# Kernel tuning notes

Measured on AMD Instinct MI355X. Metric: run time of the kernel, lower is better.

The kernel has to match this reference:

```python
import math
import jax, jax.numpy as jnp
import numpy as np

B, T, D = 4, 4096, 2048
D_MEM, H, D_HEAD = 1024, 16, 64
TABLE = 131072          # rows per head
K, DIL = 4, 2           # kernel_size, dilation = max_ngram
EPS_QK = float(np.finfo(np.float32).eps)  # nn.RMSNorm default eps
EPS_CONV = 1e-5


def _rmsnorm(x, gamma, eps):
    ms = jnp.mean(jnp.square(x), axis=-1, keepdims=True)
    return x * jax.lax.rsqrt(ms + eps) * gamma


def setup_inputs() -> dict:
    key = jax.random.key(0)
    ks = jax.random.split(key, 8)
    hidden_states = jax.random.normal(ks[0], (B, T, D), dtype=jnp.float32)
    hash_ids = jax.random.randint(ks[1], (B, T, H), 0, TABLE, dtype=jnp.int32)
    emb_table = jax.random.normal(ks[2], (H * TABLE, D_HEAD), dtype=jnp.float32) * 0.02
    key_W = jax.random.normal(ks[3], (D, D_MEM), dtype=jnp.float32) * (1.0 / math.sqrt(D_MEM))
    key_b = jnp.zeros((D,), dtype=jnp.float32)
    value_W = jax.random.normal(ks[4], (D, D_MEM), dtype=jnp.float32) * (1.0 / math.sqrt(D_MEM))
    value_b = jnp.zeros((D,), dtype=jnp.float32)
    q_gamma = jnp.ones((D,), dtype=jnp.float32)
    k_gamma = jnp.ones((D,), dtype=jnp.float32)
    cnorm_gamma = jnp.ones((D,), dtype=jnp.float32)
    conv_w = jax.random.normal(ks[5], (D, 1, K), dtype=jnp.float32) * 0.1
    return dict(hidden_states=hidden_states, hash_ids=hash_ids, emb_table=emb_table,
                key_W=key_W, key_b=key_b, value_W=value_W, value_b=value_b,
                q_gamma=q_gamma, k_gamma=k_gamma, cnorm_gamma=cnorm_gamma, conv_w=conv_w)


def reference(hidden_states, hash_ids, emb_table, key_W, key_b, value_W, value_b,
              q_gamma, k_gamma, cnorm_gamma, conv_w):
    # --- MultiHeadEmbedding: per-head offset into a single fused table ---
    offsets = (jnp.arange(H, dtype=hash_ids.dtype) * TABLE)  # [H]
    shifted = hash_ids + offsets                              # [B,T,H]
    e = emb_table[shifted].reshape(B, T, D_MEM)               # gather + flatten heads

    # --- key / value projections (torch Linear: x @ W.T + b) ---
    k = jnp.einsum('btm,dm->btd', e, key_W) + key_b
    v = jnp.einsum('btm,dm->btd', e, value_W) + value_b

    # --- RMSNorm q and k, dot-product gate (in fp32, demo mode) ---
    qn = _rmsnorm(hidden_states, q_gamma, EPS_QK)
    kn = _rmsnorm(k, k_gamma, EPS_QK)
    dot = jnp.sum(qn * kn, axis=-1) / math.sqrt(D)            # [B,T]
    dot = jnp.sqrt(jnp.maximum(jnp.abs(dot), 1e-6)) * jnp.sign(dot)  # demo gating
    gate = jax.nn.sigmoid(dot)[..., None]                     # [B,T,1]
    gated_v = gate * v                                        # [B,T,D]

    # --- ShortDepthwiseCausalConv: RMSNorm -> depthwise causal conv -> SiLU ---
    yn = _rmsnorm(gated_v, cnorm_gamma, EPS_CONV)
    yn_t = jnp.transpose(yn, (0, 2, 1))                       # [B,D,T]
    left_pad = (K - 1) * DIL
    yc = jax.lax.conv_general_dilated(
        yn_t, conv_w, window_strides=(1,), padding=[(left_pad, 0)],
        rhs_dilation=(DIL,), feature_group_count=D,
        dimension_numbers=('NCH', 'OIH', 'NCH'))              # [B,D,T]
    y = jnp.transpose(jax.nn.silu(yc), (0, 2, 1))             # [B,T,D]
    return y + gated_v
```

## Files before the change

### kernel.cpp

```cpp
#include <hip/hip_runtime.h>
#include <hip/hip_bf16.h>
#include <math.h>

#define B_      4
#define T_      4096
#define D_      2048
#define DMEM_   1024
#define H_      16
#define TABLE_  131072
#define NTOK    (B_ * T_)
#define NKV     (2 * D_)
#define NT_TILES 16
#define EPS_QK  1.1920928955078125e-07f
#define EPS_CONV 1e-5f
#define INV_D   (1.0f / 2048.0f)
#define INV_SQRT_D 0.02209708691207961f

typedef __attribute__((ext_vector_type(8))) __bf16 bf16x8;
typedef __attribute__((ext_vector_type(4))) float  f32x4;
typedef __attribute__((ext_vector_type(8))) unsigned short u16x8;

typedef __attribute__((address_space(3))) unsigned int       lds_u32;
typedef const __attribute__((address_space(1))) unsigned int glb_u32;

__device__ __forceinline__ unsigned short f2bf(float f) {
    unsigned u = __float_as_uint(f);
    u += 0x7fff + ((u >> 16) & 1);
    return (unsigned short)(u >> 16);
}
__device__ __forceinline__ float bf2f(unsigned short u) {
    return __uint_as_float(((unsigned)u) << 16);
}
__device__ __forceinline__ void gload16(const void* g, void* l) {
    __builtin_amdgcn_global_load_lds((glb_u32*)g, (lds_u32*)l, 16, 0, 0);
}

#define DSHR(x, n) __int_as_float(__builtin_amdgcn_update_dpp( \
    0, __float_as_int(x), 0x110 + (n), 0xf, 0xf, false))
#define RED16(x) do { x += DSHR(x, 1); x += DSHR(x, 2); \
                      x += DSHR(x, 4); x += DSHR(x, 8); } while (0)

__global__ __launch_bounds__(256) void prep(
    const int* __restrict__ hash_ids, const float* __restrict__ table,
    const float* __restrict__ kW, const float* __restrict__ vW,
    const float* __restrict__ kb, const float* __restrict__ vb,
    const float* __restrict__ qg, const float* __restrict__ kg,
    unsigned short* __restrict__ e, unsigned short* __restrict__ Wp,
    float* __restrict__ biasP, float* __restrict__ qkg,
    float* __restrict__ gstats )
{
    const int bid = blockIdx.x;
    const int tid = threadIdx.x;
    if (bid < NTOK) {
        const int m = tid * 4;
        const int h = m >> 6;
        const int w = m & 63;
        const long long row = (long long)hash_ids[bid * H_ + h] + (long long)h * TABLE_;
        const float4 v = *(const float4*)(table + (size_t)row * 64 + w);
        ushort4 o;
        o.x = f2bf(v.x); o.y = f2bf(v.y); o.z = f2bf(v.z); o.w = f2bf(v.w);
        *(ushort4*)(e + (size_t)bid * DMEM_ + m) = o;
    } else {
        const int n = bid - NTOK;
        const int m = tid * 4;
        const float* src = (n < D_) ? (kW + (size_t)n * DMEM_) : (vW + (size_t)(n - D_) * DMEM_);
        const float4 v = *(const float4*)(src + m);
        ushort4 o;
        o.x = f2bf(v.x); o.y = f2bf(v.y); o.z = f2bf(v.z); o.w = f2bf(v.w);
        *(ushort4*)(Wp + (size_t)n * DMEM_ + m) = o;
        if (tid == 0) biasP[n] = (n < D_) ? kb[n] : vb[n - D_];
        if (tid == 1 && n < D_) qkg[n] = qg[n] * kg[n];
        if (tid >= 16 && tid < 32) gstats[n * 16 + (tid - 16)] = 0.0f;
    }
}

#define STAGE_A(dd, mh, ts) do { \
    if ((ts) < NT_TILES) { \
        _Pragma("unroll") \
        for (int c_ = 0; c_ < 2; ++c_) { \
            const int lin_ = c_ * 512 + tid; \
            const int lr_ = lin_ >> 3, c16_ = lin_ & 7; \
            gload16(Ab + (size_t)((lr_ >> 6) * 128 + (mh) * 64 + (lr_ & 63)) * 2048 \
                       + (ts) * 128 + ((c16_ ^ (lr_ & 7)) << 4), \
                    lds + (dd) * 32768 + (mh) * 16384 + (c_ * 512 + wid * 64) * 16); \
        } \
    } \
} while (0)

#define STAGE_B(dd, nh, ts) do { \
    if ((ts) < NT_TILES) { \
        _Pragma("unroll") \
        for (int c_ = 0; c_ < 2; ++c_) { \
            const int lin_ = c_ * 512 + tid; \
            const int lr_ = lin_ >> 3, c16_ = lin_ & 7; \
            gload16(Wb + (size_t)((lr_ >> 5) * 64 + (nh) * 32 + (lr_ & 31)) * 2048 \
                       + (ts) * 128 + ((c16_ ^ (lr_ & 7)) << 4), \
                    lds + 65536 + (dd) * 32768 + (nh) * 16384 + (c_ * 512 + wid * 64) * 16); \
        } \
    } \
} while (0)

#define LDA(dd, mh) do { \
    _Pragma("unroll") \
    for (int mi_ = 0; mi_ < 4; ++mi_) { \
        const int l_ = (mh) * 128 + wm * 64 + mi_ * 16 + (lane & 15); \
        _Pragma("unroll") \
        for (int kk_ = 0; kk_ < 2; ++kk_) { \
            const int kb_ = (kk_ * 64 + ((lane >> 4) << 4)) ^ ((lane & 7) << 4); \
            af[mi_][kk_] = *(const bf16x8*)(lds + (dd) * 32768 + l_ * 128 + kb_); \
        } \
    } \
} while (0)

#define LDB(dd, nh) do { \
    _Pragma("unroll") \
    for (int ni_ = 0; ni_ < 2; ++ni_) { \
        const int l_ = (nh) * 128 + wn * 32 + ni_ * 16 + (lane & 15); \
        _Pragma("unroll") \
        for (int kk_ = 0; kk_ < 2; ++kk_) { \
            const int kb_ = (kk_ * 64 + ((lane >> 4) << 4)) ^ ((lane & 7) << 4); \
            bfr[ni_][kk_] = *(const bf16x8*)(lds + 65536 + (dd) * 32768 + l_ * 128 + kb_); \
        } \
    } \
} while (0)

#define MM(mh, nh) do { \
    __builtin_amdgcn_s_setprio(1); \
    _Pragma("unroll") \
    for (int mi_ = 0; mi_ < 4; ++mi_) \
        _Pragma("unroll") \
        for (int ni_ = 0; ni_ < 2; ++ni_) \
            _Pragma("unroll") \
            for (int kk_ = 0; kk_ < 2; ++kk_) \
                acc[(mh) * 4 + mi_][(nh) * 2 + ni_] = \
                    __builtin_amdgcn_mfma_f32_16x16x32_bf16(af[mi_][kk_], bfr[ni_][kk_], \
                        acc[(mh) * 4 + mi_][(nh) * 2 + ni_], 0, 0, 0); \
    __builtin_amdgcn_s_setprio(0); \
} while (0)

#define BAR()  do { __builtin_amdgcn_sched_barrier(0); __builtin_amdgcn_s_barrier(); __builtin_amdgcn_sched_barrier(0); } while (0)
#define BARW() do { __builtin_amdgcn_sched_barrier(0); asm volatile("s_waitcnt lgkmcnt(0)" ::: "memory"); __builtin_amdgcn_s_barrier(); __builtin_amdgcn_sched_barrier(0); } while (0)
#define VMC(n) asm volatile("s_waitcnt vmcnt(" #n ")" ::: "memory")

#define K_TILE(dd, t) do { \
    bf16x8 af[4][2]; bf16x8 bfr[2][2]; \
    LDA(dd, 0); LDB(dd, 0); STAGE_B((dd) ^ 1, 0, (t) + 1); \
    BAR(); MM(0, 0); BAR(); \
    LDB(dd, 1); STAGE_A(dd, 0, (t) + 2); \
    BAR(); MM(0, 1); BAR(); \
    LDA(dd, 1); STAGE_B(dd, 1, (t) + 2); \
    BAR(); MM(1, 1); BAR(); \
    LDB(dd, 0); STAGE_A(dd, 1, (t) + 2); \
    VMC(6); BAR(); MM(1, 0); BAR(); \
} while (0)

__global__ __launch_bounds__(512, 2) void gemm_kv(
    const unsigned short* __restrict__ A,
    const unsigned short* __restrict__ W,
    const float* __restrict__ biasP,
    const float* __restrict__ qkg,
    const float* __restrict__ hid,
    unsigned short* __restrict__ vbuf,
    float* __restrict__ gh2, float* __restrict__ gk2,
    float* __restrict__ ghk, float* __restrict__ gv2)
{
    __shared__ __align__(16) char lds[131072];
    const int tid  = threadIdx.x;
    const int wid  = tid >> 6;
    const int lane = tid & 63;
    const int bid  = blockIdx.x;
    const int swz  = (bid & 7) * 128 + (bid >> 3);
    const int bm = swz >> 4, bn = swz & 15;
    const int wm = wid >> 2, wn = wid & 3;
    const int r0 = bm * 256, c0 = bn * 256;

    const char* Ab = (const char*)A + (size_t)r0 * 2048;
    const char* Wb = (const char*)W + (size_t)c0 * 2048;

    f32x4 acc[8][4] = {};

    STAGE_A(0, 0, 0); STAGE_B(0, 0, 0); STAGE_B(0, 1, 0); STAGE_A(0, 1, 0);
    STAGE_A(1, 0, 1); STAGE_B(1, 1, 1); STAGE_A(1, 1, 1);
    VMC(6);
    BAR();

    for (int t = 0; t < NT_TILES; t += 2) {
        K_TILE(0, t);
        K_TILE(1, t + 1);
    }

    VMC(0);
    BARW();

    float breg[4];
#pragma unroll
    for (int ni = 0; ni < 4; ++ni)
        breg[ni] = biasP[c0 + wn * 64 + ni * 16 + (lane & 15)];

    if (bn < 8) {
        float* sH  = (float*)lds;
        float* sK  = sH + 256;
        float* sHK = sK + 256;
        for (int i = tid; i < 768; i += 512) sH[i] = 0.0f;
        float qreg[4];
#pragma unroll
        for (int ni = 0; ni < 4; ++ni)
            qreg[ni] = qkg[c0 + wn * 64 + ni * 16 + (lane & 15)];
        BARW();

#pragma unroll
        for (int mi = 0; mi < 8; ++mi) {
            float h2[4] = {}, k2[4] = {}, hk[4] = {};
#pragma unroll
            for (int ni = 0; ni < 4; ++ni) {
#pragma unroll
                for (int j = 0; j < 4; ++j) {
                    const float kv = acc[mi][ni][j] + breg[ni];
                    const int rl = wm * 128 + mi * 16 + (lane >> 4) * 4 + j;
                    const float hv = hid[(size_t)(r0 + rl) * 2048 + c0
                                         + wn * 64 + ni * 16 + (lane & 15)];
                    h2[j] += hv * hv;
                    k2[j] += kv * kv;
                    hk[j] += hv * qreg[ni] * kv;
                }
            }
#pragma unroll
            for (int j = 0; j < 4; ++j) {
                RED16(h2[j]); RED16(k2[j]); RED16(hk[j]);
            }
            if ((lane & 15) == 15) {
#pragma unroll
                for (int j = 0; j < 4; ++j) {
                    const int rl = wm * 128 + mi * 16 + (lane >> 4) * 4 + j;
                    atomicAdd(&sH[rl], h2[j]);
                    atomicAdd(&sK[rl], k2[j]);
                    atomicAdd(&sHK[rl], hk[j]);
                }
            }
        }
        BARW();
        if (tid < 256) {
            atomicAdd(&gh2[r0 + tid], sH[tid]);
            atomicAdd(&gk2[r0 + tid], sK[tid]);
            atomicAdd(&ghk[r0 + tid], sHK[tid]);
        }
    } else {
        float* sV = (float*)(lds + 65536);
        for (int i = tid; i < 256; i += 512) sV[i] = 0.0f;
        BARW();
        const int cv0 = (bn - 8) * 256;

#pragma unroll
        for (int mi = 0; mi < 8; ++mi) {
            float v2[4] = {};
#pragma unroll
            for (int ni = 0; ni < 4; ++ni)
#pragma unroll
                for (int j = 0; j < 4; ++j) {
                    const float vv = acc[mi][ni][j] + breg[ni];
                    v2[j] += vv * vv;
                }
#pragma unroll
            for (int j = 0; j < 4; ++j) RED16(v2[j]);
            if ((lane & 15) == 15) {
#pragma unroll
                for (int j = 0; j < 4; ++j) {
                    const int rl = wm * 128 + mi * 16 + (lane >> 4) * 4 + j;
                    atomicAdd(&sV[rl], v2[j]);
                }
            }
#pragma unroll
            for (int ni = 0; ni < 4; ++ni) {
#pragma unroll
                for (int j = 0; j < 4; ++j) {
                    const int srow = wm * 16 + (lane >> 4) * 4 + j;
                    const int colb = (wn * 64 + ni * 16 + (lane & 15)) * 2;
                    *(unsigned short*)(lds + srow * 512 + (colb ^ (((srow >> 2) & 3) << 5))) =
                        f2bf(acc[mi][ni][j] + breg[ni]);
                }
            }
            BARW();
#pragma unroll
            for (int c2 = 0; c2 < 4; ++c2) {
                const int lin = c2 * 512 + tid;
                const int srow = lin >> 6, cb8 = (lin & 63) * 8;
                const ushort4 vv = *(const ushort4*)(lds + srow * 512 + (cb8 ^ (((srow >> 2) & 3) << 5)));
                const int grow = r0 + (srow >> 4) * 128 + mi * 16 + (srow & 15);
                const int gcol = cv0 + (lin & 63) * 4;
                *(ushort4*)((char*)vbuf + (size_t)grow * 4096 + gcol * 2) = vv;
            }
            BARW();
        }
        if (tid < 256) atomicAdd(&gv2[r0 + tid], sV[tid]);
    }
}

__global__ __launch_bounds__(256) void finalize(
    const float* __restrict__ gh2, const float* __restrict__ gk2,
    const float* __restrict__ ghk, const float* __restrict__ gv2,
    float* __restrict__ gateb, float* __restrict__ grb)
{
    const int i = blockIdx.x * 256 + threadIdx.x;
    const float dot = ghk[i] * rsqrtf(gh2[i] * INV_D + EPS_QK)
                             * rsqrtf(gk2[i] * INV_D + EPS_QK) * INV_SQRT_D;
    const float sgn = (dot > 0.f) ? 1.f : ((dot < 0.f) ? -1.f : 0.f);
    const float dd = sqrtf(fmaxf(fabsf(dot), 1e-6f)) * sgn;
    const float g = 1.f / (1.f + expf(-dd));
    gateb[i] = g;
    grb[i] = g * rsqrtf(g * g * (gv2[i] * INV_D) + EPS_CONV);
}

__global__ __launch_bounds__(256) void convout(
    const unsigned short* __restrict__ vbuf,
    const float* __restrict__ gateb, const float* __restrict__ grb,
    const float* __restrict__ cg, const float* __restrict__ convw,
    float* __restrict__ out)
{
    __shared__ __align__(16) char vlds[22 * 512];
    const int bid = blockIdx.x;
    const int by = bid >> 3, bx = bid & 7;
    const int R0 = by * 16, C0 = bx * 256;
    const int tid = threadIdx.x;

#pragma unroll
    for (int c = 0; c < 3; ++c) {
        const int wbase = c * 4096 + (tid >> 6) * 1024;
        if (wbase < 11264) {
            const int off = c * 4096 + tid * 16;
            const int i = off >> 9;
            int g = R0 - 6 + i; if (g < 0) g = 0;
            gload16((const char*)vbuf + (size_t)g * 4096 + C0 * 2 + (off & 511),
                    vlds + wbase);
        }
    }
    VMC(0);
    __syncthreads();

    const int cgrp = tid & 31;
    const int rgrp = tid >> 5;
    const int dcol = C0 + cgrp * 8;
    const int cb = cgrp * 16;

    const float4 ca = *(const float4*)(cg + dcol), cbv = *(const float4*)(cg + dcol + 4);
    const float cgv[8] = {ca.x, ca.y, ca.z, ca.w, cbv.x, cbv.y, cbv.z, cbv.w};
    float w[8][4];
#pragma unroll
    for (int ee = 0; ee < 8; ++ee) {
        const float4 wv = *(const float4*)(convw + (size_t)(dcol + ee) * 4);
        w[ee][0] = wv.x; w[ee][1] = wv.y; w[ee][2] = wv.z; w[ee][3] = wv.w;
    }

#pragma unroll
    for (int rr = 0; rr < 2; ++rr) {
        const int rloc = rgrp * 2 + rr;
        const int row = R0 + rloc;
        const int t = row & (T_ - 1);
        const float g0 = gateb[row];

        float acc[8] = {};
#pragma unroll
        for (int j = 0; j < 4; ++j) {
            const int tau = t - 6 + 2 * j;
            if (tau < 0) continue;
            const float s = grb[row - 6 + 2 * j];
            const u16x8 vv = *(const u16x8*)(vlds + (rloc + 2 * j) * 512 + cb);
#pragma unroll
            for (int ee = 0; ee < 8; ++ee)
                acc[ee] += w[ee][j] * s * cgv[ee] * bf2f(vv[ee]);
        }

        const u16x8 vown = *(const u16x8*)(vlds + (rloc + 6) * 512 + cb);
        float o[8];
#pragma unroll
        for (int ee = 0; ee < 8; ++ee)
            o[ee] = acc[ee] / (1.f + expf(-acc[ee])) + g0 * bf2f(vown[ee]);

        float* op = out + (size_t)row * D_ + dcol;
        *(float4*)op       = make_float4(o[0], o[1], o[2], o[3]);
        *(float4*)(op + 4) = make_float4(o[4], o[5], o[6], o[7]);
    }
}

extern "C" void kernel_launch(void* const* d_in, const int* in_sizes, int n_in,
                              void* d_out, int out_size, void* d_ws, size_t ws_size,
                              hipStream_t stream) {
    const float* hid   = (const float*)d_in[0];
    const int*   hash  = (const int*)  d_in[1];
    const float* table = (const float*)d_in[2];
    const float* kW    = (const float*)d_in[3];
    const float* kb    = (const float*)d_in[4];
    const float* vW    = (const float*)d_in[5];
    const float* vb    = (const float*)d_in[6];
    const float* qg    = (const float*)d_in[7];
    const float* kg    = (const float*)d_in[8];
    const float* cg    = (const float*)d_in[9];
    const float* cw    = (const float*)d_in[10];
    float* out = (float*)d_out;

    char* ws = (char*)d_ws;
    unsigned short* e     = (unsigned short*)(ws);
    unsigned short* Wp    = (unsigned short*)(ws + 33554432);
    float*          biasP = (float*)(ws + 41943040);
    float*          qkg   = (float*)(ws + 41959424);
    unsigned short* vbuf  = (unsigned short*)(ws + 41967616);
    float*          gh2   = (float*)(ws + 109076480);
    float*          gk2   = (float*)(ws + 109142016);
    float*          ghk   = (float*)(ws + 109207552);
    float*          gv2   = (float*)(ws + 109273088);
    float*          gateb = (float*)(ws + 109338624);
    float*          grb   = (float*)(ws + 109404160);

    prep<<<dim3(NTOK + NKV), dim3(256), 0, stream>>>(hash, table, kW, vW, kb, vb,
                                                     qg, kg, e, Wp, biasP, qkg, gh2);
    gemm_kv<<<dim3(1024), dim3(512), 0, stream>>>(e, Wp, biasP, qkg, hid, vbuf,
                                                  gh2, gk2, ghk, gv2);
    finalize<<<dim3(64), dim3(256), 0, stream>>>(gh2, gk2, ghk, gv2, gateb, grb);
    convout<<<dim3(8192), dim3(256), 0, stream>>>(vbuf, gateb, grb, cg, cw, out);
}
```

Baseline: 250.8 us.

## Make GEMM blocks persistent over four N tiles and fuse finalize into convout

The GEMM grid shrinks from 1024 to 256 blocks. Each block loops over four consecutive 256-column N tiles that reuse the same A rows, and it prefetches the next tile's W slices during the tail of the current K loop so the pipeline does not drain between tiles. The finalize kernel is removed: each convout block now computes the gate and norm scale for its rows (plus halo) in shared memory. Convout blocks grow to 32 rows to amortize the 6-row halo. The V sum-of-squares now uses global atomics directly instead of a shared-memory reduction, so there is more global atomic traffic. With only 256 persistent blocks, parallelism is reduced.

Measured after the change: 810.1 us. 223% more time.

```diff
diff --git a/kernel.cpp b/kernel.cpp
--- a/kernel.cpp
+++ b/kernel.cpp
@@ -75,26 +75,29 @@
 }
 
 #define STAGE_A(dd, mh, ts) do { \
-    if ((ts) < NT_TILES) { \
+    if ((ts) < NT_TILES || wrapok) { \
+        const int tsw_ = (ts) & 15; \
         _Pragma("unroll") \
         for (int c_ = 0; c_ < 2; ++c_) { \
             const int lin_ = c_ * 512 + tid; \
             const int lr_ = lin_ >> 3, c16_ = lin_ & 7; \
             gload16(Ab + (size_t)((lr_ >> 6) * 128 + (mh) * 64 + (lr_ & 63)) * 2048 \
-                       + (ts) * 128 + ((c16_ ^ (lr_ & 7)) << 4), \
+                       + tsw_ * 128 + ((c16_ ^ (lr_ & 7)) << 4), \
                     lds + (dd) * 32768 + (mh) * 16384 + (c_ * 512 + wid * 64) * 16); \
         } \
     } \
 } while (0)
 
 #define STAGE_B(dd, nh, ts) do { \
-    if ((ts) < NT_TILES) { \
+    if ((ts) < NT_TILES || wrapok) { \
+        const int tsw_ = (ts) & 15; \
+        const char* wp_ = ((ts) < NT_TILES) ? Wb : Wbn; \
         _Pragma("unroll") \
         for (int c_ = 0; c_ < 2; ++c_) { \
             const int lin_ = c_ * 512 + tid; \
             const int lr_ = lin_ >> 3, c16_ = lin_ & 7; \
-            gload16(Wb + (size_t)((lr_ >> 5) * 64 + (nh) * 32 + (lr_ & 31)) * 2048 \
-                       + (ts) * 128 + ((c16_ ^ (lr_ & 7)) << 4), \
+            gload16(wp_ + (size_t)((lr_ >> 5) * 64 + (nh) * 32 + (lr_ & 31)) * 2048 \
+                       + tsw_ * 128 + ((c16_ ^ (lr_ & 7)) << 4), \
                     lds + 65536 + (dd) * 32768 + (nh) * 16384 + (c_ * 512 + wid * 64) * 16); \
         } \
     } \
@@ -169,167 +172,174 @@
     const int wid  = tid >> 6;
     const int lane = tid & 63;
     const int bid  = blockIdx.x;
-    const int swz  = (bid & 7) * 128 + (bid >> 3);
-    const int bm = swz >> 4, bn = swz & 15;
+    const int j8   = bid >> 3;
+    const int bm   = (bid & 7) * 8 + (j8 >> 2);
+    const int g    = j8 & 3;
     const int wm = wid >> 2, wn = wid & 3;
-    const int r0 = bm * 256, c0 = bn * 256;
-
-    const char* Ab = (const char*)A + (size_t)r0 * 2048;
-    const char* Wb = (const char*)W + (size_t)c0 * 2048;
-
-    f32x4 acc[8][4] = {};
-
-    STAGE_A(0, 0, 0); STAGE_B(0, 0, 0); STAGE_B(0, 1, 0); STAGE_A(0, 1, 0);
-    STAGE_A(1, 0, 1); STAGE_B(1, 1, 1); STAGE_A(1, 1, 1);
-    VMC(6);
-    BAR();
-
-    for (int t = 0; t < NT_TILES; t += 2) {
-        K_TILE(0, t);
-        K_TILE(1, t + 1);
-    }
-
-    VMC(0);
-    BARW();
-
-    float breg[4];
-#pragma unroll
-    for (int ni = 0; ni < 4; ++ni)
-        breg[ni] = biasP[c0 + wn * 64 + ni * 16 + (lane & 15)];
-
-    if (bn < 8) {
-        float* sH  = (float*)lds;
-        float* sK  = sH + 256;
-        float* sHK = sK + 256;
-        for (int i = tid; i < 768; i += 512) sH[i] = 0.0f;
-        float qreg[4];
+    const int r0 = bm * 256;
+
+    const char* Ab    = (const char*)A + (size_t)r0 * 2048;
+    const char* Wbase = (const char*)W;
+
+    for (int cc = 0; cc < 4; ++cc) {
+        const int bn = g * 4 + cc;
+        const int c0 = bn * 256;
+        const char* Wb  = Wbase + (size_t)c0 * 2048;
+        const char* Wbn = Wbase + (size_t)(c0 + 256) * 2048;
+        const int wrapok = (cc < 3);
+
+        f32x4 acc[8][4] = {};
+
+        if (cc == 0) {
+            STAGE_A(0, 0, 0); STAGE_B(0, 0, 0); STAGE_B(0, 1, 0); STAGE_A(0, 1, 0);
+            STAGE_A(1, 0, 1); STAGE_B(1, 1, 1); STAGE_A(1, 1, 1);
+            VMC(6);
+            BAR();
+        }
+
+        for (int t = 0; t < NT_TILES; t += 2) {
+            K_TILE(0, t);
+            K_TILE(1, t + 1);
+        }
+
+        float breg[4];
 #pragma unroll
         for (int ni = 0; ni < 4; ++ni)
-            qreg[ni] = qkg[c0 + wn * 64 + ni * 16 + (lane & 15)];
-        BARW();
-
-#pragma unroll
-        for (int mi = 0; mi < 8; ++mi) {
-            float h2[4] = {}, k2[4] = {}, hk[4] = {};
-#pragma unroll
-            for (int ni = 0; ni < 4; ++ni) {
+            breg[ni] = biasP[c0 + wn * 64 + ni * 16 + (lane & 15)];
+
+        if (g < 2) {
+            float* sH  = (float*)(lds + 98304);
+            float* sK  = sH + 256;
+            float* sHK = sK + 256;
+            for (int i = tid; i < 768; i += 512) sH[i] = 0.0f;
+            float qreg[4];
+#pragma unroll
+            for (int ni = 0; ni < 4; ++ni)
+                qreg[ni] = qkg[c0 + wn * 64 + ni * 16 + (lane & 15)];
+            BARW();
+
+#pragma unroll
+            for (int mi = 0; mi < 8; ++mi) {
+                float h2[4] = {}, k2[4] = {}, hk[4] = {};
+#pragma unroll
+                for (int ni = 0; ni < 4; ++ni) {
+#pragma unroll
+                    for (int j = 0; j < 4; ++j) {
+                        const float kv = acc[mi][ni][j] + breg[ni];
+                        const int rl = wm * 128 + mi * 16 + (lane >> 4) * 4 + j;
+                        const float hv = hid[(size_t)(r0 + rl) * 2048 + c0
+                                             + wn * 64 + ni * 16 + (lane & 15)];
+                        h2[j] += hv * hv;
+                        k2[j] += kv * kv;
+                        hk[j] += hv * qreg[ni] * kv;
+                    }
+                }
 #pragma unroll
                 for (int j = 0; j < 4; ++j) {
-                    const float kv = acc[mi][ni][j] + breg[ni];
-                    const int rl = wm * 128 + mi * 16 + (lane >> 4) * 4 + j;
-                    const float hv = hid[(size_t)(r0 + rl) * 2048 + c0
-                                         + wn * 64 + ni * 16 + (lane & 15)];
-                    h2[j] += hv * hv;
-                    k2[j] += kv * kv;
-                    hk[j] += hv * qreg[ni] * kv;
+                    RED16(h2[j]); RED16(k2[j]); RED16(hk[j]);
+                }
+                if ((lane & 15) == 15) {
+#pragma unroll
+                    for (int j = 0; j < 4; ++j) {
+                        const int rl = wm * 128 + mi * 16 + (lane >> 4) * 4 + j;
+                        atomicAdd(&sH[rl], h2[j]);
+                        atomicAdd(&sK[rl], k2[j]);
+                        atomicAdd(&sHK[rl], hk[j]);
+                    }
                 }
             }
-#pragma unroll
-            for (int j = 0; j < 4; ++j) {
-                RED16(h2[j]); RED16(k2[j]); RED16(hk[j]);
+            BARW();
+            if (tid < 256) {
+                atomicAdd(&gh2[r0 + tid], sH[tid]);
+                atomicAdd(&gk2[r0 + tid], sK[tid]);
+                atomicAdd(&ghk[r0 + tid], sHK[tid]);
             }
-            if ((lane & 15) == 15) {
-#pragma unroll
-                for (int j = 0; j < 4; ++j) {
-                    const int rl = wm * 128 + mi * 16 + (lane >> 4) * 4 + j;
-                    atomicAdd(&sH[rl], h2[j]);
-                    atomicAdd(&sK[rl], k2[j]);
-                    atomicAdd(&sHK[rl], hk[j]);
-                }
+        } else {
+            char* slab = lds + 98304;
+            const int cv0 = (bn - 8) * 256;
+
+#pragma unroll
+            for (int mi = 0; mi < 8; ++mi) {
+                float v2[4] = {};
+#pragma unroll
+                for (int ni = 0; ni < 4; ++ni)
+#pragma unroll
+                    for (int j = 0; j < 4; ++j) {
+                        const float vv = acc[mi][ni][j] + breg[ni];
+                        v2[j] += vv * vv;
+                    }
+#pragma unroll
+                for (int j = 0; j < 4; ++j) RED16(v2[j]);
+                if ((lane & 15) == 15) {
+#pragma unroll
+                    for (int j = 0; j < 4; ++j) {
+                        const int rl = wm * 128 + mi * 16 + (lane >> 4) * 4 + j;
+                        atomicAdd(&gv2[r0 + rl], v2[j]);
+                    }
+                }
+#pragma unroll
+                for (int ni = 0; ni < 4; ++ni) {
+#pragma unroll
+                    for (int j = 0; j < 4; ++j) {
+                        const int srow = wm * 16 + (lane >> 4) * 4 + j;
+                        const int colb = (wn * 64 + ni * 16 + (lane & 15)) * 2;
+                        *(unsigned short*)(slab + srow * 512 + (colb ^ (((srow >> 2) & 3) << 5))) =
+                            f2bf(acc[mi][ni][j] + breg[ni]);
+                    }
+                }
+                BARW();
+#pragma unroll
+                for (int c2 = 0; c2 < 4; ++c2) {
+                    const int lin = c2 * 512 + tid;
+                    const int srow = lin >> 6, cb8 = (lin & 63) * 8;
+                    const ushort4 vv = *(const ushort4*)(slab + srow * 512 + (cb8 ^ (((srow >> 2) & 3) << 5)));
+                    const int grow = r0 + (srow >> 4) * 128 + mi * 16 + (srow & 15);
+                    const int gcol = cv0 + (lin & 63) * 4;
+                    *(ushort4*)((char*)vbuf + (size_t)grow * 4096 + gcol * 2) = vv;
+                }
+                BARW();
             }
         }
+
+        VMC(0);
         BARW();
-        if (tid < 256) {
-            atomicAdd(&gh2[r0 + tid], sH[tid]);
-            atomicAdd(&gk2[r0 + tid], sK[tid]);
-            atomicAdd(&ghk[r0 + tid], sHK[tid]);
-        }
-    } else {
-        float* sV = (float*)(lds + 65536);
-        for (int i = tid; i < 256; i += 512) sV[i] = 0.0f;
-        BARW();
-        const int cv0 = (bn - 8) * 256;
-
-#pragma unroll
-        for (int mi = 0; mi < 8; ++mi) {
-            float v2[4] = {};
-#pragma unroll
-            for (int ni = 0; ni < 4; ++ni)
-#pragma unroll
-                for (int j = 0; j < 4; ++j) {
-                    const float vv = acc[mi][ni][j] + breg[ni];
-                    v2[j] += vv * vv;
-                }
-#pragma unroll
-            for (int j = 0; j < 4; ++j) RED16(v2[j]);
-            if ((lane & 15) == 15) {
-#pragma unroll
-                for (int j = 0; j < 4; ++j) {
-                    const int rl = wm * 128 + mi * 16 + (lane >> 4) * 4 + j;
-                    atomicAdd(&sV[rl], v2[j]);
-                }
-            }
-#pragma unroll
-            for (int ni = 0; ni < 4; ++ni) {
-#pragma unroll
-                for (int j = 0; j < 4; ++j) {
-                    const int srow = wm * 16 + (lane >> 4) * 4 + j;
-                    const int colb = (wn * 64 + ni * 16 + (lane & 15)) * 2;
-                    *(unsigned short*)(lds + srow * 512 + (colb ^ (((srow >> 2) & 3) << 5))) =
-                        f2bf(acc[mi][ni][j] + breg[ni]);
-                }
-            }
-            BARW();
-#pragma unroll
-            for (int c2 = 0; c2 < 4; ++c2) {
-                const int lin = c2 * 512 + tid;
-                const int srow = lin >> 6, cb8 = (lin & 63) * 8;
-                const ushort4 vv = *(const ushort4*)(lds + srow * 512 + (cb8 ^ (((srow >> 2) & 3) << 5)));
-                const int grow = r0 + (srow >> 4) * 128 + mi * 16 + (srow & 15);
-                const int gcol = cv0 + (lin & 63) * 4;
-                *(ushort4*)((char*)vbuf + (size_t)grow * 4096 + gcol * 2) = vv;
-            }
-            BARW();
-        }
-        if (tid < 256) atomicAdd(&gv2[r0 + tid], sV[tid]);
-    }
-}
-
-__global__ __launch_bounds__(256) void finalize(
+    }
+}
+
+__global__ __launch_bounds__(256) void convout(
+    const unsigned short* __restrict__ vbuf,
     const float* __restrict__ gh2, const float* __restrict__ gk2,
     const float* __restrict__ ghk, const float* __restrict__ gv2,
-    float* __restrict__ gateb, float* __restrict__ grb)
-{
-    const int i = blockIdx.x * 256 + threadIdx.x;
-    const float dot = ghk[i] * rsqrtf(gh2[i] * INV_D + EPS_QK)
-                             * rsqrtf(gk2[i] * INV_D + EPS_QK) * INV_SQRT_D;
-    const float sgn = (dot > 0.f) ? 1.f : ((dot < 0.f) ? -1.f : 0.f);
-    const float dd = sqrtf(fmaxf(fabsf(dot), 1e-6f)) * sgn;
-    const float g = 1.f / (1.f + expf(-dd));
-    gateb[i] = g;
-    grb[i] = g * rsqrtf(g * g * (gv2[i] * INV_D) + EPS_CONV);
-}
-
-__global__ __launch_bounds__(256) void convout(
-    const unsigned short* __restrict__ vbuf,
-    const float* __restrict__ gateb, const float* __restrict__ grb,
     const float* __restrict__ cg, const float* __restrict__ convw,
     float* __restrict__ out)
 {
-    __shared__ __align__(16) char vlds[22 * 512];
+    __shared__ __align__(16) char vlds[38 * 512];
+    __shared__ float sgate[38];
+    __shared__ float sgr[38];
     const int bid = blockIdx.x;
     const int by = bid >> 3, bx = bid & 7;
-    const int R0 = by * 16, C0 = bx * 256;
+    const int R0 = by * 32, C0 = bx * 256;
     const int tid = threadIdx.x;
 
-#pragma unroll
-    for (int c = 0; c < 3; ++c) {
+    if (tid < 38) {
+        int r = R0 - 6 + tid; if (r < 0) r = 0;
+        const float dot = ghk[r] * rsqrtf(gh2[r] * INV_D + EPS_QK)
+                                 * rsqrtf(gk2[r] * INV_D + EPS_QK) * INV_SQRT_D;
+        const float sgn = (dot > 0.f) ? 1.f : ((dot < 0.f) ? -1.f : 0.f);
+        const float dd = sqrtf(fmaxf(fabsf(dot), 1e-6f)) * sgn;
+        const float gg = 1.f / (1.f + expf(-dd));
+        sgate[tid] = gg;
+        sgr[tid]   = gg * rsqrtf(gg * gg * (gv2[r] * INV_D) + EPS_CONV);
+    }
+
+#pragma unroll
+    for (int c = 0; c < 5; ++c) {
         const int wbase = c * 4096 + (tid >> 6) * 1024;
-        if (wbase < 11264) {
+        if (wbase < 19456) {
             const int off = c * 4096 + tid * 16;
             const int i = off >> 9;
-            int g = R0 - 6 + i; if (g < 0) g = 0;
-            gload16((const char*)vbuf + (size_t)g * 4096 + C0 * 2 + (off & 511),
+            int gsrc = R0 - 6 + i; if (gsrc < 0) gsrc = 0;
+            gload16((const char*)vbuf + (size_t)gsrc * 4096 + C0 * 2 + (off & 511),
                     vlds + wbase);
         }
     }
@@ -351,18 +361,18 @@
     }
 
 #pragma unroll
-    for (int rr = 0; rr < 2; ++rr) {
-        const int rloc = rgrp * 2 + rr;
+    for (int rr = 0; rr < 4; ++rr) {
+        const int rloc = rgrp * 4 + rr;
         const int row = R0 + rloc;
         const int t = row & (T_ - 1);
-        const float g0 = gateb[row];
+        const float g0 = sgate[rloc + 6];
 
         float acc[8] = {};
 #pragma unroll
         for (int j = 0; j < 4; ++j) {
             const int tau = t - 6 + 2 * j;
             if (tau < 0) continue;
-            const float s = grb[row - 6 + 2 * j];
+            const float s = sgr[rloc + 2 * j];
             const u16x8 vv = *(const u16x8*)(vlds + (rloc + 2 * j) * 512 + cb);
 #pragma unroll
             for (int ee = 0; ee < 8; ++ee)
@@ -407,13 +417,11 @@
     float*          gk2   = (float*)(ws + 109142016);
     float*          ghk   = (float*)(ws + 109207552);
     float*          gv2   = (float*)(ws + 109273088);
-    float*          gateb = (float*)(ws + 109338624);
-    float*          grb   = (float*)(ws + 109404160);
 
     prep<<<dim3(NTOK + NKV), dim3(256), 0, stream>>>(hash, table, kW, vW, kb, vb,
                                                      qg, kg, e, Wp, biasP, qkg, gh2);
-    gemm_kv<<<dim3(1024), dim3(512), 0, stream>>>(e, Wp, biasP, qkg, hid, vbuf,
-                                                  gh2, gk2, ghk, gv2);
-    finalize<<<dim3(64), dim3(256), 0, stream>>>(gh2, gk2, ghk, gv2, gateb, grb);
-    convout<<<dim3(8192), dim3(256), 0, stream>>>(vbuf, gateb, grb, cg, cw, out);
-}
+    gemm_kv<<<dim3(256), dim3(512), 0, stream>>>(e, Wp, biasP, qkg, hid, vbuf,
+                                                 gh2, gk2, ghk, gv2);
+    convout<<<dim3(4096), dim3(256), 0, stream>>>(vbuf, gh2, gk2, ghk, gv2,
+                                                  cg, cw, out);
+}
```

## Fuse gate finalize into convout and double conv rows per block

Applied to the files above, without the earlier changes.

Removes the separate finalize kernel by having each convout block recompute the gate and conv-norm scale for its 38 needed rows into shared memory. Convout now processes 32 rows per block instead of 16, which cuts halo reload overhead and halves the grid. The GEMM main loop's last tile pair is peeled with an extra full wait and barrier before the final tile. The goals are to save a kernel launch plus a global round trip and to reduce redundant halo loads. The cost is some redundant gate computation and more LDS per block.

Result: faster. 230.6 us, median of 2 (-8.1%).

```diff
diff --git a/kernel.cpp b/kernel.cpp
--- a/kernel.cpp
+++ b/kernel.cpp
@@ -184,10 +184,14 @@
     VMC(6);
     BAR();
 
-    for (int t = 0; t < NT_TILES; t += 2) {
+    for (int t = 0; t < NT_TILES - 2; t += 2) {
         K_TILE(0, t);
         K_TILE(1, t + 1);
     }
+    K_TILE(0, NT_TILES - 2);
+    VMC(0);
+    BAR();
+    K_TILE(1, NT_TILES - 1);
 
     VMC(0);
     BARW();
@@ -295,41 +299,40 @@
     }
 }
 
-__global__ __launch_bounds__(256) void finalize(
+__global__ __launch_bounds__(256) void convout(
+    const unsigned short* __restrict__ vbuf,
     const float* __restrict__ gh2, const float* __restrict__ gk2,
     const float* __restrict__ ghk, const float* __restrict__ gv2,
-    float* __restrict__ gateb, float* __restrict__ grb)
-{
-    const int i = blockIdx.x * 256 + threadIdx.x;
-    const float dot = ghk[i] * rsqrtf(gh2[i] * INV_D + EPS_QK)
-                             * rsqrtf(gk2[i] * INV_D + EPS_QK) * INV_SQRT_D;
-    const float sgn = (dot > 0.f) ? 1.f : ((dot < 0.f) ? -1.f : 0.f);
-    const float dd = sqrtf(fmaxf(fabsf(dot), 1e-6f)) * sgn;
-    const float g = 1.f / (1.f + expf(-dd));
-    gateb[i] = g;
-    grb[i] = g * rsqrtf(g * g * (gv2[i] * INV_D) + EPS_CONV);
-}
-
-__global__ __launch_bounds__(256) void convout(
-    const unsigned short* __restrict__ vbuf,
-    const float* __restrict__ gateb, const float* __restrict__ grb,
     const float* __restrict__ cg, const float* __restrict__ convw,
     float* __restrict__ out)
 {
-    __shared__ __align__(16) char vlds[22 * 512];
+    __shared__ __align__(16) char vlds[38 * 512];
+    __shared__ float sgate[38];
+    __shared__ float sgr[38];
     const int bid = blockIdx.x;
     const int by = bid >> 3, bx = bid & 7;
-    const int R0 = by * 16, C0 = bx * 256;
+    const int R0 = by * 32, C0 = bx * 256;
     const int tid = threadIdx.x;
 
-#pragma unroll
-    for (int c = 0; c < 3; ++c) {
+    if (tid < 38) {
+        int r = R0 - 6 + tid; if (r < 0) r = 0;
+        const float dot = ghk[r] * rsqrtf(gh2[r] * INV_D + EPS_QK)
+                                 * rsqrtf(gk2[r] * INV_D + EPS_QK) * INV_SQRT_D;
+        const float sgn = (dot > 0.f) ? 1.f : ((dot < 0.f) ? -1.f : 0.f);
+        const float dd = sqrtf(fmaxf(fabsf(dot), 1e-6f)) * sgn;
+        const float gg = 1.f / (1.f + expf(-dd));
+        sgate[tid] = gg;
+        sgr[tid]   = gg * rsqrtf(gg * gg * (gv2[r] * INV_D) + EPS_CONV);
+    }
+
+#pragma unroll
+    for (int c = 0; c < 5; ++c) {
         const int wbase = c * 4096 + (tid >> 6) * 1024;
-        if (wbase < 11264) {
+        if (wbase < 19456) {
             const int off = c * 4096 + tid * 16;
             const int i = off >> 9;
-            int g = R0 - 6 + i; if (g < 0) g = 0;
-            gload16((const char*)vbuf + (size_t)g * 4096 + C0 * 2 + (off & 511),
+            int gsrc = R0 - 6 + i; if (gsrc < 0) gsrc = 0;
+            gload16((const char*)vbuf + (size_t)gsrc * 4096 + C0 * 2 + (off & 511),
                     vlds + wbase);
         }
     }
@@ -351,18 +354,18 @@
     }
 
 #pragma unroll
-    for (int rr = 0; rr < 2; ++rr) {
-        const int rloc = rgrp * 2 + rr;
+    for (int rr = 0; rr < 4; ++rr) {
+        const int rloc = rgrp * 4 + rr;
         const int row = R0 + rloc;
         const int t = row & (T_ - 1);
-        const float g0 = gateb[row];
+        const float g0 = sgate[rloc + 6];
 
         float acc[8] = {};
 #pragma unroll
         for (int j = 0; j < 4; ++j) {
             const int tau = t - 6 + 2 * j;
             if (tau < 0) continue;
-            const float s = grb[row - 6 + 2 * j];
+            const float s = sgr[rloc + 2 * j];
             const u16x8 vv = *(const u16x8*)(vlds + (rloc + 2 * j) * 512 + cb);
 #pragma unroll
             for (int ee = 0; ee < 8; ++ee)
@@ -407,13 +410,11 @@
     float*          gk2   = (float*)(ws + 109142016);
     float*          ghk   = (float*)(ws + 109207552);
     float*          gv2   = (float*)(ws + 109273088);
-    float*          gateb = (float*)(ws + 109338624);
-    float*          grb   = (float*)(ws + 109404160);
 
     prep<<<dim3(NTOK + NKV), dim3(256), 0, stream>>>(hash, table, kW, vW, kb, vb,
                                                      qg, kg, e, Wp, biasP, qkg, gh2);
     gemm_kv<<<dim3(1024), dim3(512), 0, stream>>>(e, Wp, biasP, qkg, hid, vbuf,
                                                   gh2, gk2, ghk, gv2);
-    finalize<<<dim3(64), dim3(256), 0, stream>>>(gh2, gk2, ghk, gv2, gateb, grb);
-    convout<<<dim3(8192), dim3(256), 0, stream>>>(vbuf, gateb, grb, cg, cw, out);
-}
+    convout<<<dim3(4096), dim3(256), 0, stream>>>(vbuf, gh2, gk2, ghk, gv2,
+                                                  cg, cw, out);
+}
```
